# Optimization experiments

Measured on AMD Instinct MI355X. Metric: run time of the kernel, lower is better.

## Reference

```python
import jax, jax.numpy as jnp
import numpy as np

EMBED_DIM = 64
B, H, S, D = 2, 16, 2048, EMBED_DIM


def setup_inputs() -> dict:
    key = jax.random.key(0)
    ks = jax.random.split(key, 5)
    shp = (B, H, S, D)
    return {
        "Q": jax.random.normal(ks[0], shp, dtype=jnp.float32),
        "K": jax.random.normal(ks[1], shp, dtype=jnp.float32),
        "V": jax.random.normal(ks[2], shp, dtype=jnp.float32),
        "Q_position": jax.random.normal(ks[3], shp, dtype=jnp.float32),
        "K_position": jax.random.normal(ks[4], shp, dtype=jnp.float32),
    }


def reference(Q, K, V, Q_position, K_position):
    scale = 1.0 / np.sqrt(EMBED_DIM).astype(np.float32)
    # content scores + positional similarity, both scaled by 1/sqrt(d)
    scores = jnp.einsum("bhqd,bhkd->bhqk", Q, K) * scale
    scores = scores + jnp.einsum("bhqd,bhkd->bhqk", Q_position, K_position) * scale
    attn = jax.nn.softmax(scores, axis=-1)
    context = jnp.einsum("bhqk,bhkd->bhqd", attn, V)
    return context
```

## Files before the change

kernel.cpp:

```cpp
#include <hip/hip_runtime.h>

#define BH_ 32
#define S_ 2048
#define D_ 64
#define DQK 128
#define BQ 256

typedef unsigned short u16;
typedef unsigned int u32;
typedef u16 u16x8 __attribute__((ext_vector_type(8)));
typedef u32 u32x4 __attribute__((ext_vector_type(4)));
typedef __bf16 bf16x8 __attribute__((ext_vector_type(8)));
typedef float f32x16 __attribute__((ext_vector_type(16)));

__device__ __forceinline__ u16 f2bf_rne(float f) {
  unsigned u = __builtin_bit_cast(unsigned, f);
  u += 0x7fffu + ((u >> 16) & 1u);
  return (u16)(u >> 16);
}
__device__ __forceinline__ bf16x8 ld8(const u16* p) {
  return __builtin_bit_cast(bf16x8, *(const u16x8*)p);
}
__device__ __forceinline__ void g2l16(const u16* g, u16* l) {
  __builtin_amdgcn_global_load_lds(
      (const __attribute__((address_space(1))) unsigned int*)g,
      (__attribute__((address_space(3))) unsigned int*)l, 16, 0, 0);
}
__device__ __forceinline__ u32 cvtpk(float lo, float hi) {
  u32 r;
  asm("v_cvt_pk_bf16_f32 %0, %1, %2" : "=v"(r) : "v"(lo), "v"(hi));
  return r;
}
__device__ __forceinline__ void swap32(u32& a, u32& b) {
  asm("v_permlane32_swap_b32 %0, %1" : "+v"(a), "+v"(b));
}
__device__ __forceinline__ f32x16 zero16() {
  f32x16 z;
  #pragma unroll
  for (int i = 0; i < 16; ++i) z[i] = 0.f;
  return z;
}

#define COEF 0.1803368801111204f

__global__ __launch_bounds__(256)
void prep_kernel(const float* __restrict__ K, const float* __restrict__ V,
                 const float* __restrict__ Kp,
                 u16* __restrict__ Kc, u16* __restrict__ Vt) {
  __shared__ float Ls[64][65];
  int b = blockIdx.x;
  if (b < 4096) {
    int t = b * 256 + threadIdx.x;
    int kv    = t & 63;
    int chunk = (t >> 6) & 15;
    int kt    = (t >> 10) & 31;
    int bh    = t >> 15;
    int s     = kt * 64 + kv;
    int col8  = chunk * 8;
    const float* src = (col8 < 64) ? (K  + ((size_t)bh * S_ + s) * D_ + col8)
                                   : (Kp + ((size_t)bh * S_ + s) * D_ + (col8 - 64));
    float4 v0 = *(const float4*)src;
    float4 v1 = *(const float4*)(src + 4);
    u16x8 w;
    w[0] = f2bf_rne(v0.x); w[1] = f2bf_rne(v0.y); w[2] = f2bf_rne(v0.z); w[3] = f2bf_rne(v0.w);
    w[4] = f2bf_rne(v1.x); w[5] = f2bf_rne(v1.y); w[6] = f2bf_rne(v1.z); w[7] = f2bf_rne(v1.w);
    *(u16x8*)(Kc + ((((size_t)bh * 32 + kt) * 16 + chunk) * 64 + kv) * 8) = w;
  } else {
    int id = b - 4096;
    int bh = id >> 5, kt = id & 31;
    int tid = threadIdx.x;
    #pragma unroll
    for (int it = 0; it < 4; ++it) {
      int i = it * 256 + tid;
      int kv = i >> 4, dg = (i & 15) * 4;
      float4 v = *(const float4*)(V + ((size_t)bh * S_ + kt * 64 + kv) * D_ + dg);
      Ls[kv][dg + 0] = v.x; Ls[kv][dg + 1] = v.y;
      Ls[kv][dg + 2] = v.z; Ls[kv][dg + 3] = v.w;
    }
    __syncthreads();
    int d = tid >> 2, kvg = (tid & 3) * 16;
    u16x8 w0, w1;
    #pragma unroll
    for (int j = 0; j < 8; ++j) w0[j] = f2bf_rne(Ls[kvg + j][d]);
    #pragma unroll
    for (int j = 0; j < 8; ++j) w1[j] = f2bf_rne(Ls[kvg + 8 + j][d]);
    u16* base = Vt + ((size_t)bh * 32 + kt) * 4096;
    int c = (tid & 3) * 2;
    *(u16x8*)(base + ((size_t)(c * 64 + d)) * 8)       = w0;
    *(u16x8*)(base + ((size_t)((c + 1) * 64 + d)) * 8) = w1;
  }
}

template <int SPLIT>
__global__ __launch_bounds__(256, 2)
void fa3_kernel(const float* __restrict__ Q, const float* __restrict__ Qp,
                const u16* __restrict__ Kc, const u16* __restrict__ Vtg,
                float* __restrict__ out, float* __restrict__ Opart,
                float* __restrict__ lpart) {
  __shared__ alignas(16) u16 Ks[3][8192];
  __shared__ alignas(16) u16 Vs[3][4096];

  const int tid  = threadIdx.x;
  const int wave = tid >> 6;
  const int lane = tid & 63;
  const int l32  = lane & 31;
  const int hi   = lane >> 5;

  const int id   = blockIdx.x;
  const int p    = SPLIT ? (id & 63) : (id & 31);
  const int qblk = SPLIT ? (id >> 6) : (id >> 5);
  const int bh   = p & 31;
  const int kz   = SPLIT ? (p >> 5) : 0;

  const int qw = qblk * BQ + wave * 64;
  const int kt0 = kz * 16;
  const int NKT = SPLIT ? 16 : 32;

  bf16x8 bq[2][8];
  #pragma unroll
  for (int g = 0; g < 2; ++g)
    #pragma unroll
    for (int kstep = 0; kstep < 8; ++kstep) {
      int k0 = kstep * 16 + hi * 8;
      const float* src = (k0 < 64)
          ? (Q  + ((size_t)bh * S_ + qw + g * 32 + l32) * D_ + k0)
          : (Qp + ((size_t)bh * S_ + qw + g * 32 + l32) * D_ + (k0 - 64));
      float4 v0 = *(const float4*)src;
      float4 v1 = *(const float4*)(src + 4);
      u16x8 w;
      w[0] = f2bf_rne(v0.x * COEF); w[1] = f2bf_rne(v0.y * COEF);
      w[2] = f2bf_rne(v0.z * COEF); w[3] = f2bf_rne(v0.w * COEF);
      w[4] = f2bf_rne(v1.x * COEF); w[5] = f2bf_rne(v1.y * COEF);
      w[6] = f2bf_rne(v1.z * COEF); w[7] = f2bf_rne(v1.w * COEF);
      bq[g][kstep] = __builtin_bit_cast(bf16x8, w);
    }

  const u16* kcp = Kc  + ((size_t)bh * 32 + kt0) * 8192 + tid * 8;
  const u16* vtp = Vtg + ((size_t)bh * 32 + kt0) * 4096 + tid * 8;

  #pragma unroll
  for (int j = 0; j < 4; ++j) g2l16(kcp + j * 2048, &Ks[0][0] + tid * 8 + j * 2048);
  #pragma unroll
  for (int j = 0; j < 2; ++j) g2l16(vtp + j * 2048, &Vs[0][0] + tid * 8 + j * 2048);
  #pragma unroll
  for (int j = 0; j < 4; ++j) g2l16(kcp + 8192 + j * 2048, &Ks[1][0] + tid * 8 + j * 2048);
  #pragma unroll
  for (int j = 0; j < 2; ++j) g2l16(vtp + 4096 + j * 2048, &Vs[1][0] + tid * 8 + j * 2048);

  f32x16 accd[2][2];
  #pragma unroll
  for (int g = 0; g < 2; ++g) { accd[g][0] = zero16(); accd[g][1] = zero16(); }
  float l_part[2] = {0.f, 0.f};

  int cur = 0;
  for (int kt = 0; kt < NKT; ++kt) {
    if (kt == NKT - 1) asm volatile("s_waitcnt vmcnt(0)" ::: "memory");
    else               asm volatile("s_waitcnt vmcnt(6)" ::: "memory");
    __builtin_amdgcn_s_barrier();
    if (kt + 2 < NKT) {
      int nx = cur + 2; if (nx >= 3) nx -= 3;
      const u16* kg = kcp + (size_t)(kt + 2) * 8192;
      u16* kl = &Ks[nx][0] + tid * 8;
      #pragma unroll
      for (int j = 0; j < 4; ++j) g2l16(kg + j * 2048, kl + j * 2048);
      const u16* vg = vtp + (size_t)(kt + 2) * 4096;
      u16* vl = &Vs[nx][0] + tid * 8;
      #pragma unroll
      for (int j = 0; j < 2; ++j) g2l16(vg + j * 2048, vl + j * 2048);
    }
    __builtin_amdgcn_sched_barrier(0);

    const u16* ksb = &Ks[cur][0];
    const u16* vsb = &Vs[cur][0];

    f32x16 s[2][2];
    #pragma unroll
    for (int g = 0; g < 2; ++g) { s[g][0] = zero16(); s[g][1] = zero16(); }
    #pragma unroll
    for (int kstep = 0; kstep < 8; ++kstep) {
      bf16x8 akA = ld8(ksb + (((kstep * 2 + hi) * 64) + l32) * 8);
      bf16x8 akB = ld8(ksb + (((kstep * 2 + hi) * 64) + 32 + l32) * 8);
      #pragma unroll
      for (int g = 0; g < 2; ++g) {
        s[g][0] = __builtin_amdgcn_mfma_f32_32x32x16_bf16(akA, bq[g][kstep], s[g][0], 0, 0, 0);
        s[g][1] = __builtin_amdgcn_mfma_f32_32x32x16_bf16(akB, bq[g][kstep], s[g][1], 0, 0, 0);
      }
    }

    #pragma unroll
    for (int h = 0; h < 2; ++h) {
      #pragma unroll
      for (int g = 0; g < 2; ++g) {
        float rs0 = 0.f, rs1 = 0.f;
        #pragma unroll
        for (int r = 0; r < 8; ++r) {
          float e0 = __builtin_amdgcn_exp2f(s[g][h][r]);
          float e1 = __builtin_amdgcn_exp2f(s[g][h][8 + r]);
          s[g][h][r] = e0; s[g][h][8 + r] = e1;
          rs0 += e0; rs1 += e1;
        }
        l_part[g] += rs0 + rs1;
      }
      #pragma unroll
      for (int k2 = 0; k2 < 2; ++k2) {
        bf16x8 pa[2];
        #pragma unroll
        for (int g = 0; g < 2; ++g) {
          u32 a0 = cvtpk(s[g][h][8 * k2 + 0], s[g][h][8 * k2 + 1]);
          u32 b0 = cvtpk(s[g][h][8 * k2 + 4], s[g][h][8 * k2 + 5]);
          swap32(a0, b0);
          u32 a1 = cvtpk(s[g][h][8 * k2 + 2], s[g][h][8 * k2 + 3]);
          u32 b1 = cvtpk(s[g][h][8 * k2 + 6], s[g][h][8 * k2 + 7]);
          swap32(a1, b1);
          u32x4 pw; pw[0] = a0; pw[1] = a1; pw[2] = b0; pw[3] = b1;
          pa[g] = __builtin_bit_cast(bf16x8, pw);
        }
        int ksl = 2 * h + k2;
        #pragma unroll
        for (int dt = 0; dt < 2; ++dt) {
          bf16x8 bv = ld8(vsb + (((ksl * 2 + hi) * 64) + dt * 32 + l32) * 8);
          #pragma unroll
          for (int g = 0; g < 2; ++g)
            accd[g][dt] = __builtin_amdgcn_mfma_f32_32x32x16_bf16(pa[g], bv, accd[g][dt], 0, 0, 0);
        }
      }
    }
    cur = (cur == 2) ? 0 : cur + 1;
  }

  #pragma unroll
  for (int g = 0; g < 2; ++g) {
    float lsum = l_part[g] + __shfl_xor(l_part[g], 32);
    if (SPLIT) {
      #pragma unroll
      for (int r = 0; r < 16; ++r) {
        int qrow = (r & 3) + 8 * (r >> 2) + 4 * hi;
        size_t rowb = ((size_t)kz * 65536 + (size_t)bh * S_ + qw + g * 32 + qrow) * D_;
        Opart[rowb + l32]      = accd[g][0][r];
        Opart[rowb + 32 + l32] = accd[g][1][r];
      }
      if (hi == 0)
        lpart[(size_t)kz * 65536 + (size_t)bh * S_ + qw + g * 32 + l32] = lsum;
    } else {
      #pragma unroll
      for (int r = 0; r < 16; ++r) {
        int qrow = (r & 3) + 8 * (r >> 2) + 4 * hi;
        float inv = 1.0f / __shfl(lsum, qrow);
        size_t rowb = ((size_t)bh * S_ + qw + g * 32 + qrow) * D_;
        out[rowb + l32]      = accd[g][0][r] * inv;
        out[rowb + 32 + l32] = accd[g][1][r] * inv;
      }
    }
  }
}

__global__ __launch_bounds__(256)
void combine_kernel(const float* __restrict__ Opart, const float* __restrict__ lpart,
                    float* __restrict__ out) {
  int t = blockIdx.x * 256 + threadIdx.x;
  int row = t >> 4;
  int d4  = (t & 15) * 4;
  float4 o0 = *(const float4*)(Opart + (size_t)row * D_ + d4);
  float4 o1 = *(const float4*)(Opart + (size_t)65536 * D_ + (size_t)row * D_ + d4);
  float inv = 1.0f / (lpart[row] + lpart[65536 + row]);
  float4 o;
  o.x = (o0.x + o1.x) * inv; o.y = (o0.y + o1.y) * inv;
  o.z = (o0.z + o1.z) * inv; o.w = (o0.w + o1.w) * inv;
  *(float4*)(out + (size_t)row * D_ + d4) = o;
}

extern "C" void kernel_launch(void* const* d_in, const int* in_sizes, int n_in,
                              void* d_out, int out_size, void* d_ws, size_t ws_size,
                              hipStream_t stream) {
  const float* Q  = (const float*)d_in[0];
  const float* K  = (const float*)d_in[1];
  const float* V  = (const float*)d_in[2];
  const float* Qp = (const float*)d_in[3];
  const float* Kp = (const float*)d_in[4];
  float* out = (float*)d_out;

  const size_t nKc = (size_t)BH_ * S_ * DQK;
  const size_t nVt = (size_t)BH_ * S_ * D_;
  const size_t nO  = (size_t)2 * 65536 * D_;
  const size_t nL  = (size_t)2 * 65536;
  const size_t needSplit = (nO + nL) * 4 + (nKc + nVt) * 2;

  if (ws_size >= needSplit) {
    float* Opart = (float*)d_ws;
    float* lpart = Opart + nO;
    u16* Kc = (u16*)(lpart + nL);
    u16* Vt = Kc + nKc;
    prep_kernel<<<dim3(4096 + 1024), dim3(256), 0, stream>>>(K, V, Kp, Kc, Vt);
    fa3_kernel<1><<<dim3((S_ / BQ) * BH_ * 2), dim3(256), 0, stream>>>(Q, Qp, Kc, Vt, nullptr, Opart, lpart);
    combine_kernel<<<dim3(4096), dim3(256), 0, stream>>>(Opart, lpart, out);
  } else {
    u16* Kc = (u16*)d_ws;
    u16* Vt = Kc + nKc;
    prep_kernel<<<dim3(4096 + 1024), dim3(256), 0, stream>>>(K, V, Kp, Kc, Vt);
    fa3_kernel<0><<<dim3((S_ / BQ) * BH_), dim3(256), 0, stream>>>(Q, Qp, Kc, Vt, out, nullptr, nullptr);
  }
}
```

Before: 176.6 us.

## Interleave exp2 softmax work with MFMA chains and add setprio around matrix phases

Restructures the per-tile inner loop so that the QK^T MFMAs for the second key half run while the exp2 work for the first half executes. The exp2 work for the second half is likewise interleaved with the PV MFMAs of the first half. s_setprio raises wave priority around the pure MFMA phases. The aim is to hide transcendental VALU latency behind matrix-core work instead of running the two phases back to back. This relies on the compiler preserving the interleaving, and the row-sum accumulation order changes slightly.

```diff
diff --git a/kernel.cpp b/kernel.cpp
--- a/kernel.cpp
+++ b/kernel.cpp
@@ -39,6 +39,17 @@
   #pragma unroll
   for (int i = 0; i < 16; ++i) z[i] = 0.f;
   return z;
+}
+__device__ __forceinline__ bf16x8 mkfrag(float s0, float s1, float s2, float s3,
+                                         float s4, float s5, float s6, float s7) {
+  u32 a0 = cvtpk(s0, s1);
+  u32 b0 = cvtpk(s4, s5);
+  swap32(a0, b0);
+  u32 a1 = cvtpk(s2, s3);
+  u32 b1 = cvtpk(s6, s7);
+  swap32(a1, b1);
+  u32x4 pw; pw[0] = a0; pw[1] = a1; pw[2] = b0; pw[3] = b1;
+  return __builtin_bit_cast(bf16x8, pw);
 }
 
 #define COEF 0.1803368801111204f
@@ -173,58 +184,84 @@
     const u16* ksb = &Ks[cur][0];
     const u16* vsb = &Vs[cur][0];
 
-    f32x16 s[2][2];
-    #pragma unroll
-    for (int g = 0; g < 2; ++g) { s[g][0] = zero16(); s[g][1] = zero16(); }
+    f32x16 s0g0 = zero16(), s0g1 = zero16();
+    f32x16 s1g0 = zero16(), s1g1 = zero16();
+    __builtin_amdgcn_s_setprio(1);
     #pragma unroll
     for (int kstep = 0; kstep < 8; ++kstep) {
       bf16x8 akA = ld8(ksb + (((kstep * 2 + hi) * 64) + l32) * 8);
+      s0g0 = __builtin_amdgcn_mfma_f32_32x32x16_bf16(akA, bq[0][kstep], s0g0, 0, 0, 0);
+      s0g1 = __builtin_amdgcn_mfma_f32_32x32x16_bf16(akA, bq[1][kstep], s0g1, 0, 0, 0);
+    }
+    __builtin_amdgcn_s_setprio(0);
+
+    float rs00 = 0.f, rs01 = 0.f, rs10 = 0.f, rs11 = 0.f;
+    #pragma unroll
+    for (int kstep = 0; kstep < 8; ++kstep) {
       bf16x8 akB = ld8(ksb + (((kstep * 2 + hi) * 64) + 32 + l32) * 8);
-      #pragma unroll
-      for (int g = 0; g < 2; ++g) {
-        s[g][0] = __builtin_amdgcn_mfma_f32_32x32x16_bf16(akA, bq[g][kstep], s[g][0], 0, 0, 0);
-        s[g][1] = __builtin_amdgcn_mfma_f32_32x32x16_bf16(akB, bq[g][kstep], s[g][1], 0, 0, 0);
+      s1g0 = __builtin_amdgcn_mfma_f32_32x32x16_bf16(akB, bq[0][kstep], s1g0, 0, 0, 0);
+      s1g1 = __builtin_amdgcn_mfma_f32_32x32x16_bf16(akB, bq[1][kstep], s1g1, 0, 0, 0);
+      const int r0 = kstep * 2, r1 = kstep * 2 + 1;
+      float e;
+      e = __builtin_amdgcn_exp2f(s0g0[r0]); s0g0[r0] = e; rs00 += e;
+      e = __builtin_amdgcn_exp2f(s0g0[r1]); s0g0[r1] = e; rs01 += e;
+      e = __builtin_amdgcn_exp2f(s0g1[r0]); s0g1[r0] = e; rs10 += e;
+      e = __builtin_amdgcn_exp2f(s0g1[r1]); s0g1[r1] = e; rs11 += e;
+    }
+    l_part[0] += rs00 + rs01;
+    l_part[1] += rs10 + rs11;
+
+    bf16x8 paA[2], paB[2];
+    #pragma unroll
+    for (int k2 = 0; k2 < 2; ++k2) {
+      paA[k2] = mkfrag(s0g0[8 * k2 + 0], s0g0[8 * k2 + 1], s0g0[8 * k2 + 2], s0g0[8 * k2 + 3],
+                       s0g0[8 * k2 + 4], s0g0[8 * k2 + 5], s0g0[8 * k2 + 6], s0g0[8 * k2 + 7]);
+      paB[k2] = mkfrag(s0g1[8 * k2 + 0], s0g1[8 * k2 + 1], s0g1[8 * k2 + 2], s0g1[8 * k2 + 3],
+                       s0g1[8 * k2 + 4], s0g1[8 * k2 + 5], s0g1[8 * k2 + 6], s0g1[8 * k2 + 7]);
+    }
+
+    float ts00 = 0.f, ts01 = 0.f, ts10 = 0.f, ts11 = 0.f;
+    #pragma unroll
+    for (int k2 = 0; k2 < 2; ++k2) {
+      #pragma unroll
+      for (int dt = 0; dt < 2; ++dt) {
+        bf16x8 bv = ld8(vsb + (((k2 * 2 + hi) * 64) + dt * 32 + l32) * 8);
+        accd[0][dt] = __builtin_amdgcn_mfma_f32_32x32x16_bf16(paA[k2], bv, accd[0][dt], 0, 0, 0);
+        accd[1][dt] = __builtin_amdgcn_mfma_f32_32x32x16_bf16(paB[k2], bv, accd[1][dt], 0, 0, 0);
+        const int rb = k2 * 8 + dt * 4;
+        float e;
+        e = __builtin_amdgcn_exp2f(s1g0[rb + 0]); s1g0[rb + 0] = e; ts00 += e;
+        e = __builtin_amdgcn_exp2f(s1g0[rb + 1]); s1g0[rb + 1] = e; ts01 += e;
+        e = __builtin_amdgcn_exp2f(s1g0[rb + 2]); s1g0[rb + 2] = e; ts00 += e;
+        e = __builtin_amdgcn_exp2f(s1g0[rb + 3]); s1g0[rb + 3] = e; ts01 += e;
+        e = __builtin_amdgcn_exp2f(s1g1[rb + 0]); s1g1[rb + 0] = e; ts10 += e;
+        e = __builtin_amdgcn_exp2f(s1g1[rb + 1]); s1g1[rb + 1] = e; ts11 += e;
+        e = __builtin_amdgcn_exp2f(s1g1[rb + 2]); s1g1[rb + 2] = e; ts10 += e;
+        e = __builtin_amdgcn_exp2f(s1g1[rb + 3]); s1g1[rb + 3] = e; ts11 += e;
       }
     }
-
-    #pragma unroll
-    for (int h = 0; h < 2; ++h) {
-      #pragma unroll
-      for (int g = 0; g < 2; ++g) {
-        float rs0 = 0.f, rs1 = 0.f;
-        #pragma unroll
-        for (int r = 0; r < 8; ++r) {
-          float e0 = __builtin_amdgcn_exp2f(s[g][h][r]);
-          float e1 = __builtin_amdgcn_exp2f(s[g][h][8 + r]);
-          s[g][h][r] = e0; s[g][h][8 + r] = e1;
-          rs0 += e0; rs1 += e1;
-        }
-        l_part[g] += rs0 + rs1;
+    l_part[0] += ts00 + ts01;
+    l_part[1] += ts10 + ts11;
+
+    #pragma unroll
+    for (int k2 = 0; k2 < 2; ++k2) {
+      paA[k2] = mkfrag(s1g0[8 * k2 + 0], s1g0[8 * k2 + 1], s1g0[8 * k2 + 2], s1g0[8 * k2 + 3],
+                       s1g0[8 * k2 + 4], s1g0[8 * k2 + 5], s1g0[8 * k2 + 6], s1g0[8 * k2 + 7]);
+      paB[k2] = mkfrag(s1g1[8 * k2 + 0], s1g1[8 * k2 + 1], s1g1[8 * k2 + 2], s1g1[8 * k2 + 3],
+                       s1g1[8 * k2 + 4], s1g1[8 * k2 + 5], s1g1[8 * k2 + 6], s1g1[8 * k2 + 7]);
+    }
+    __builtin_amdgcn_s_setprio(1);
+    #pragma unroll
+    for (int k2 = 0; k2 < 2; ++k2) {
+      #pragma unroll
+      for (int dt = 0; dt < 2; ++dt) {
+        bf16x8 bv = ld8(vsb + ((((2 + k2) * 2 + hi) * 64) + dt * 32 + l32) * 8);
+        accd[0][dt] = __builtin_amdgcn_mfma_f32_32x32x16_bf16(paA[k2], bv, accd[0][dt], 0, 0, 0);
+        accd[1][dt] = __builtin_amdgcn_mfma_f32_32x32x16_bf16(paB[k2], bv, accd[1][dt], 0, 0, 0);
       }
-      #pragma unroll
-      for (int k2 = 0; k2 < 2; ++k2) {
-        bf16x8 pa[2];
-        #pragma unroll
-        for (int g = 0; g < 2; ++g) {
-          u32 a0 = cvtpk(s[g][h][8 * k2 + 0], s[g][h][8 * k2 + 1]);
-          u32 b0 = cvtpk(s[g][h][8 * k2 + 4], s[g][h][8 * k2 + 5]);
-          swap32(a0, b0);
-          u32 a1 = cvtpk(s[g][h][8 * k2 + 2], s[g][h][8 * k2 + 3]);
-          u32 b1 = cvtpk(s[g][h][8 * k2 + 6], s[g][h][8 * k2 + 7]);
-          swap32(a1, b1);
-          u32x4 pw; pw[0] = a0; pw[1] = a1; pw[2] = b0; pw[3] = b1;
-          pa[g] = __builtin_bit_cast(bf16x8, pw);
-        }
-        int ksl = 2 * h + k2;
-        #pragma unroll
-        for (int dt = 0; dt < 2; ++dt) {
-          bf16x8 bv = ld8(vsb + (((ksl * 2 + hi) * 64) + dt * 32 + l32) * 8);
-          #pragma unroll
-          for (int g = 0; g < 2; ++g)
-            accd[g][dt] = __builtin_amdgcn_mfma_f32_32x32x16_bf16(pa[g], bv, accd[g][dt], 0, 0, 0);
-        }
-      }
-    }
+    }
+    __builtin_amdgcn_s_setprio(0);
+
     cur = (cur == 2) ? 0 : cur + 1;
   }
 
```

Result: no change. 178.2 us (+0.9%).

## Fuse prep, attention and combine into one cooperative kernel with grid syncs

Applied to the files above, without the earlier changes.

Replaces the three-kernel sequence (K/V bf16 conversion, split-K attention, partial combine) with a single cooperative kernel of 512 blocks that runs the three phases separated by grid-wide syncs. This removes two kernel launch boundaries and their drain/ramp gaps. In exchange, the grid is fixed at 512 blocks with 2 blocks per CU, which caps occupancy and parallelism per phase, and the grid barriers add their own cost. If the cooperative launch fails, it falls back to the old three-kernel path.

```diff
diff --git a/kernel.cpp b/kernel.cpp
--- a/kernel.cpp
+++ b/kernel.cpp
@@ -1,4 +1,7 @@
 #include <hip/hip_runtime.h>
+#include <hip/hip_cooperative_groups.h>
+
+namespace cg = cooperative_groups;
 
 #define BH_ 32
 #define S_ 2048
@@ -42,6 +45,229 @@
 }
 
 #define COEF 0.1803368801111204f
+
+__global__ __launch_bounds__(256, 2)
+void mega_kernel(const float* __restrict__ Q, const float* __restrict__ K,
+                 const float* __restrict__ V, const float* __restrict__ Qp,
+                 const float* __restrict__ Kp,
+                 u16* __restrict__ Kc, u16* __restrict__ Vtg,
+                 float* __restrict__ Opart, float* __restrict__ lpart,
+                 float* __restrict__ out) {
+  __shared__ alignas(16) u16 Ks[3][8192];
+  __shared__ alignas(16) u16 Vs[3][4096];
+
+  const int tid  = threadIdx.x;
+  const int bid  = blockIdx.x;
+  const int gtid = bid * 256 + tid;
+
+  #pragma unroll
+  for (int it = 0; it < 8; ++it) {
+    int t = it * 131072 + gtid;
+    int kv    = t & 63;
+    int chunk = (t >> 6) & 15;
+    int kt    = (t >> 10) & 31;
+    int bh    = t >> 15;
+    int s     = kt * 64 + kv;
+    int col8  = chunk * 8;
+    const float* src = (col8 < 64) ? (K  + ((size_t)bh * S_ + s) * D_ + col8)
+                                   : (Kp + ((size_t)bh * S_ + s) * D_ + (col8 - 64));
+    float4 v0 = *(const float4*)src;
+    float4 v1 = *(const float4*)(src + 4);
+    u16x8 w;
+    w[0] = f2bf_rne(v0.x); w[1] = f2bf_rne(v0.y); w[2] = f2bf_rne(v0.z); w[3] = f2bf_rne(v0.w);
+    w[4] = f2bf_rne(v1.x); w[5] = f2bf_rne(v1.y); w[6] = f2bf_rne(v1.z); w[7] = f2bf_rne(v1.w);
+    *(u16x8*)(Kc + ((((size_t)bh * 32 + kt) * 16 + chunk) * 64 + kv) * 8) = w;
+  }
+
+  {
+    float (*Ls)[65] = reinterpret_cast<float(*)[65]>(&Ks[0][0]);
+    #pragma unroll
+    for (int rep = 0; rep < 2; ++rep) {
+      int idt = bid * 2 + rep;
+      int bh = idt >> 5, kt = idt & 31;
+      __syncthreads();
+      #pragma unroll
+      for (int it = 0; it < 4; ++it) {
+        int i = it * 256 + tid;
+        int kv = i >> 4, dg = (i & 15) * 4;
+        float4 v = *(const float4*)(V + ((size_t)bh * S_ + kt * 64 + kv) * D_ + dg);
+        Ls[kv][dg + 0] = v.x; Ls[kv][dg + 1] = v.y;
+        Ls[kv][dg + 2] = v.z; Ls[kv][dg + 3] = v.w;
+      }
+      __syncthreads();
+      int d = tid >> 2, kvg = (tid & 3) * 16;
+      u16x8 w0, w1;
+      #pragma unroll
+      for (int j = 0; j < 8; ++j) w0[j] = f2bf_rne(Ls[kvg + j][d]);
+      #pragma unroll
+      for (int j = 0; j < 8; ++j) w1[j] = f2bf_rne(Ls[kvg + 8 + j][d]);
+      u16* base = Vtg + ((size_t)bh * 32 + kt) * 4096;
+      int c = (tid & 3) * 2;
+      *(u16x8*)(base + ((size_t)(c * 64 + d)) * 8)       = w0;
+      *(u16x8*)(base + ((size_t)((c + 1) * 64 + d)) * 8) = w1;
+    }
+  }
+
+  cg::this_grid().sync();
+
+  {
+    const int wave = tid >> 6;
+    const int lane = tid & 63;
+    const int l32  = lane & 31;
+    const int hi   = lane >> 5;
+
+    const int p    = bid & 63;
+    const int qblk = bid >> 6;
+    const int bh   = p & 31;
+    const int kz   = p >> 5;
+
+    const int qw = qblk * BQ + wave * 64;
+    const int kt0 = kz * 16;
+    const int NKT = 16;
+
+    bf16x8 bq[2][8];
+    #pragma unroll
+    for (int g = 0; g < 2; ++g)
+      #pragma unroll
+      for (int kstep = 0; kstep < 8; ++kstep) {
+        int k0 = kstep * 16 + hi * 8;
+        const float* src = (k0 < 64)
+            ? (Q  + ((size_t)bh * S_ + qw + g * 32 + l32) * D_ + k0)
+            : (Qp + ((size_t)bh * S_ + qw + g * 32 + l32) * D_ + (k0 - 64));
+        float4 v0 = *(const float4*)src;
+        float4 v1 = *(const float4*)(src + 4);
+        u16x8 w;
+        w[0] = f2bf_rne(v0.x * COEF); w[1] = f2bf_rne(v0.y * COEF);
+        w[2] = f2bf_rne(v0.z * COEF); w[3] = f2bf_rne(v0.w * COEF);
+        w[4] = f2bf_rne(v1.x * COEF); w[5] = f2bf_rne(v1.y * COEF);
+        w[6] = f2bf_rne(v1.z * COEF); w[7] = f2bf_rne(v1.w * COEF);
+        bq[g][kstep] = __builtin_bit_cast(bf16x8, w);
+      }
+
+    const u16* kcp = Kc  + ((size_t)bh * 32 + kt0) * 8192 + tid * 8;
+    const u16* vtp = Vtg + ((size_t)bh * 32 + kt0) * 4096 + tid * 8;
+
+    #pragma unroll
+    for (int j = 0; j < 4; ++j) g2l16(kcp + j * 2048, &Ks[0][0] + tid * 8 + j * 2048);
+    #pragma unroll
+    for (int j = 0; j < 2; ++j) g2l16(vtp + j * 2048, &Vs[0][0] + tid * 8 + j * 2048);
+    #pragma unroll
+    for (int j = 0; j < 4; ++j) g2l16(kcp + 8192 + j * 2048, &Ks[1][0] + tid * 8 + j * 2048);
+    #pragma unroll
+    for (int j = 0; j < 2; ++j) g2l16(vtp + 4096 + j * 2048, &Vs[1][0] + tid * 8 + j * 2048);
+
+    f32x16 accd[2][2];
+    #pragma unroll
+    for (int g = 0; g < 2; ++g) { accd[g][0] = zero16(); accd[g][1] = zero16(); }
+    float l_part[2] = {0.f, 0.f};
+
+    int cur = 0;
+    for (int kt = 0; kt < NKT; ++kt) {
+      if (kt == NKT - 1) asm volatile("s_waitcnt vmcnt(0)" ::: "memory");
+      else               asm volatile("s_waitcnt vmcnt(6)" ::: "memory");
+      __builtin_amdgcn_s_barrier();
+      if (kt + 2 < NKT) {
+        int nx = cur + 2; if (nx >= 3) nx -= 3;
+        const u16* kg = kcp + (size_t)(kt + 2) * 8192;
+        u16* kl = &Ks[nx][0] + tid * 8;
+        #pragma unroll
+        for (int j = 0; j < 4; ++j) g2l16(kg + j * 2048, kl + j * 2048);
+        const u16* vg = vtp + (size_t)(kt + 2) * 4096;
+        u16* vl = &Vs[nx][0] + tid * 8;
+        #pragma unroll
+        for (int j = 0; j < 2; ++j) g2l16(vg + j * 2048, vl + j * 2048);
+      }
+      __builtin_amdgcn_sched_barrier(0);
+
+      const u16* ksb = &Ks[cur][0];
+      const u16* vsb = &Vs[cur][0];
+
+      f32x16 s[2][2];
+      #pragma unroll
+      for (int g = 0; g < 2; ++g) { s[g][0] = zero16(); s[g][1] = zero16(); }
+      #pragma unroll
+      for (int kstep = 0; kstep < 8; ++kstep) {
+        bf16x8 akA = ld8(ksb + (((kstep * 2 + hi) * 64) + l32) * 8);
+        bf16x8 akB = ld8(ksb + (((kstep * 2 + hi) * 64) + 32 + l32) * 8);
+        #pragma unroll
+        for (int g = 0; g < 2; ++g) {
+          s[g][0] = __builtin_amdgcn_mfma_f32_32x32x16_bf16(akA, bq[g][kstep], s[g][0], 0, 0, 0);
+          s[g][1] = __builtin_amdgcn_mfma_f32_32x32x16_bf16(akB, bq[g][kstep], s[g][1], 0, 0, 0);
+        }
+      }
+
+      #pragma unroll
+      for (int h = 0; h < 2; ++h) {
+        #pragma unroll
+        for (int g = 0; g < 2; ++g) {
+          float rs0 = 0.f, rs1 = 0.f;
+          #pragma unroll
+          for (int r = 0; r < 8; ++r) {
+            float e0 = __builtin_amdgcn_exp2f(s[g][h][r]);
+            float e1 = __builtin_amdgcn_exp2f(s[g][h][8 + r]);
+            s[g][h][r] = e0; s[g][h][8 + r] = e1;
+            rs0 += e0; rs1 += e1;
+          }
+          l_part[g] += rs0 + rs1;
+        }
+        #pragma unroll
+        for (int k2 = 0; k2 < 2; ++k2) {
+          bf16x8 pa[2];
+          #pragma unroll
+          for (int g = 0; g < 2; ++g) {
+            u32 a0 = cvtpk(s[g][h][8 * k2 + 0], s[g][h][8 * k2 + 1]);
+            u32 b0 = cvtpk(s[g][h][8 * k2 + 4], s[g][h][8 * k2 + 5]);
+            swap32(a0, b0);
+            u32 a1 = cvtpk(s[g][h][8 * k2 + 2], s[g][h][8 * k2 + 3]);
+            u32 b1 = cvtpk(s[g][h][8 * k2 + 6], s[g][h][8 * k2 + 7]);
+            swap32(a1, b1);
+            u32x4 pw; pw[0] = a0; pw[1] = a1; pw[2] = b0; pw[3] = b1;
+            pa[g] = __builtin_bit_cast(bf16x8, pw);
+          }
+          int ksl = 2 * h + k2;
+          #pragma unroll
+          for (int dt = 0; dt < 2; ++dt) {
+            bf16x8 bv = ld8(vsb + (((ksl * 2 + hi) * 64) + dt * 32 + l32) * 8);
+            #pragma unroll
+            for (int g = 0; g < 2; ++g)
+              accd[g][dt] = __builtin_amdgcn_mfma_f32_32x32x16_bf16(pa[g], bv, accd[g][dt], 0, 0, 0);
+          }
+        }
+      }
+      cur = (cur == 2) ? 0 : cur + 1;
+    }
+
+    #pragma unroll
+    for (int g = 0; g < 2; ++g) {
+      float lsum = l_part[g] + __shfl_xor(l_part[g], 32);
+      #pragma unroll
+      for (int r = 0; r < 16; ++r) {
+        int qrow = (r & 3) + 8 * (r >> 2) + 4 * hi;
+        size_t rowb = ((size_t)kz * 65536 + (size_t)bh * S_ + qw + g * 32 + qrow) * D_;
+        Opart[rowb + l32]      = accd[g][0][r];
+        Opart[rowb + 32 + l32] = accd[g][1][r];
+      }
+      if (hi == 0)
+        lpart[(size_t)kz * 65536 + (size_t)bh * S_ + qw + g * 32 + l32] = lsum;
+    }
+  }
+
+  cg::this_grid().sync();
+
+  #pragma unroll
+  for (int it = 0; it < 8; ++it) {
+    int t = it * 131072 + gtid;
+    int row = t >> 4;
+    int d4  = (t & 15) * 4;
+    float4 o0 = *(const float4*)(Opart + (size_t)row * D_ + d4);
+    float4 o1 = *(const float4*)(Opart + (size_t)65536 * D_ + (size_t)row * D_ + d4);
+    float inv = 1.0f / (lpart[row] + lpart[65536 + row]);
+    float4 o;
+    o.x = (o0.x + o1.x) * inv; o.y = (o0.y + o1.y) * inv;
+    o.z = (o0.z + o1.z) * inv; o.w = (o0.w + o1.w) * inv;
+    *(float4*)(out + (size_t)row * D_ + d4) = o;
+  }
+}
 
 __global__ __launch_bounds__(256)
 void prep_kernel(const float* __restrict__ K, const float* __restrict__ V,
@@ -290,9 +516,18 @@
     float* lpart = Opart + nO;
     u16* Kc = (u16*)(lpart + nL);
     u16* Vt = Kc + nKc;
-    prep_kernel<<<dim3(4096 + 1024), dim3(256), 0, stream>>>(K, V, Kp, Kc, Vt);
-    fa3_kernel<1><<<dim3((S_ / BQ) * BH_ * 2), dim3(256), 0, stream>>>(Q, Qp, Kc, Vt, nullptr, Opart, lpart);
-    combine_kernel<<<dim3(4096), dim3(256), 0, stream>>>(Opart, lpart, out);
+
+    void* args[] = {(void*)&Q, (void*)&K, (void*)&V, (void*)&Qp, (void*)&Kp,
+                    (void*)&Kc, (void*)&Vt, (void*)&Opart, (void*)&lpart,
+                    (void*)&out};
+    hipError_t e = hipLaunchCooperativeKernel((const void*)mega_kernel,
+                                              dim3(512), dim3(256), args, 0, stream);
+    if (e != hipSuccess) {
+      (void)hipGetLastError();
+      prep_kernel<<<dim3(4096 + 1024), dim3(256), 0, stream>>>(K, V, Kp, Kc, Vt);
+      fa3_kernel<1><<<dim3((S_ / BQ) * BH_ * 2), dim3(256), 0, stream>>>(Q, Qp, Kc, Vt, nullptr, Opart, lpart);
+      combine_kernel<<<dim3(4096), dim3(256), 0, stream>>>(Opart, lpart, out);
+    }
   } else {
     u16* Kc = (u16*)d_ws;
     u16* Vt = Kc + nKc;
```

Result: slower. 321.6 us (+82.1%).

## Fuse split-K combine into attention kernel via per-tile atomic counter

Applied to the files above, without the earlier changes.

Removes the separate combine kernel. Each split-K block writes its partial O and row sums, then bumps an atomic counter for its (bh, qblk) pair. The second block to finish reads the other half's partials and writes the normalized output directly. This saves a kernel launch and a full reread and rewrite of the partial buffers, at the cost of a threadfence, extra syncthreads and an atomic per block. The flags are reset inside the prep kernel.

```diff
diff --git a/kernel.cpp b/kernel.cpp
--- a/kernel.cpp
+++ b/kernel.cpp
@@ -46,9 +46,11 @@
 __global__ __launch_bounds__(256)
 void prep_kernel(const float* __restrict__ K, const float* __restrict__ V,
                  const float* __restrict__ Kp,
-                 u16* __restrict__ Kc, u16* __restrict__ Vt) {
+                 u16* __restrict__ Kc, u16* __restrict__ Vt,
+                 int* __restrict__ flags) {
   __shared__ float Ls[64][65];
   int b = blockIdx.x;
+  if (b == 0 && flags != nullptr) flags[threadIdx.x] = 0;
   if (b < 4096) {
     int t = b * 256 + threadIdx.x;
     int kv    = t & 63;
@@ -96,7 +98,7 @@
 void fa3_kernel(const float* __restrict__ Q, const float* __restrict__ Qp,
                 const u16* __restrict__ Kc, const u16* __restrict__ Vtg,
                 float* __restrict__ out, float* __restrict__ Opart,
-                float* __restrict__ lpart) {
+                float* __restrict__ lpart, int* __restrict__ flags) {
   __shared__ alignas(16) u16 Ks[3][8192];
   __shared__ alignas(16) u16 Vs[3][4096];
 
@@ -228,10 +230,13 @@
     cur = (cur == 2) ? 0 : cur + 1;
   }
 
-  #pragma unroll
-  for (int g = 0; g < 2; ++g) {
-    float lsum = l_part[g] + __shfl_xor(l_part[g], 32);
-    if (SPLIT) {
+  float lsum[2];
+  #pragma unroll
+  for (int g = 0; g < 2; ++g) lsum[g] = l_part[g] + __shfl_xor(l_part[g], 32);
+
+  if (SPLIT) {
+    #pragma unroll
+    for (int g = 0; g < 2; ++g) {
       #pragma unroll
       for (int r = 0; r < 16; ++r) {
         int qrow = (r & 3) + 8 * (r >> 2) + 4 * hi;
@@ -240,33 +245,47 @@
         Opart[rowb + 32 + l32] = accd[g][1][r];
       }
       if (hi == 0)
-        lpart[(size_t)kz * 65536 + (size_t)bh * S_ + qw + g * 32 + l32] = lsum;
-    } else {
+        lpart[(size_t)kz * 65536 + (size_t)bh * S_ + qw + g * 32 + l32] = lsum[g];
+    }
+    __threadfence();
+    __syncthreads();
+    if (tid == 0) {
+      int pair = bh * (S_ / BQ) + qblk;
+      ((volatile int*)&Vs[0][0])[0] = atomicAdd(&flags[pair], 1);
+    }
+    __syncthreads();
+    int old = ((volatile int*)&Vs[0][0])[0];
+    if (old == 1) {
+      __threadfence();
+      const float* lp = lpart + (size_t)(kz ^ 1) * 65536 + (size_t)bh * S_;
+      #pragma unroll
+      for (int g = 0; g < 2; ++g) {
+        #pragma unroll
+        for (int r = 0; r < 16; ++r) {
+          int qrow = (r & 3) + 8 * (r >> 2) + 4 * hi;
+          float lo  = __shfl(lsum[g], qrow);
+          float lpv = lp[qw + g * 32 + qrow];
+          float inv = 1.0f / (lo + lpv);
+          size_t prow = ((size_t)(kz ^ 1) * 65536 + (size_t)bh * S_ + qw + g * 32 + qrow) * D_;
+          size_t orow = ((size_t)bh * S_ + qw + g * 32 + qrow) * D_;
+          out[orow + l32]      = (accd[g][0][r] + Opart[prow + l32])      * inv;
+          out[orow + 32 + l32] = (accd[g][1][r] + Opart[prow + 32 + l32]) * inv;
+        }
+      }
+    }
+  } else {
+    #pragma unroll
+    for (int g = 0; g < 2; ++g) {
       #pragma unroll
       for (int r = 0; r < 16; ++r) {
         int qrow = (r & 3) + 8 * (r >> 2) + 4 * hi;
-        float inv = 1.0f / __shfl(lsum, qrow);
+        float inv = 1.0f / __shfl(lsum[g], qrow);
         size_t rowb = ((size_t)bh * S_ + qw + g * 32 + qrow) * D_;
         out[rowb + l32]      = accd[g][0][r] * inv;
         out[rowb + 32 + l32] = accd[g][1][r] * inv;
       }
     }
   }
-}
-
-__global__ __launch_bounds__(256)
-void combine_kernel(const float* __restrict__ Opart, const float* __restrict__ lpart,
-                    float* __restrict__ out) {
-  int t = blockIdx.x * 256 + threadIdx.x;
-  int row = t >> 4;
-  int d4  = (t & 15) * 4;
-  float4 o0 = *(const float4*)(Opart + (size_t)row * D_ + d4);
-  float4 o1 = *(const float4*)(Opart + (size_t)65536 * D_ + (size_t)row * D_ + d4);
-  float inv = 1.0f / (lpart[row] + lpart[65536 + row]);
-  float4 o;
-  o.x = (o0.x + o1.x) * inv; o.y = (o0.y + o1.y) * inv;
-  o.z = (o0.z + o1.z) * inv; o.w = (o0.w + o1.w) * inv;
-  *(float4*)(out + (size_t)row * D_ + d4) = o;
 }
 
 extern "C" void kernel_launch(void* const* d_in, const int* in_sizes, int n_in,
@@ -283,20 +302,20 @@
   const size_t nVt = (size_t)BH_ * S_ * D_;
   const size_t nO  = (size_t)2 * 65536 * D_;
   const size_t nL  = (size_t)2 * 65536;
-  const size_t needSplit = (nO + nL) * 4 + (nKc + nVt) * 2;
+  const size_t needSplit = (nO + nL) * 4 + (nKc + nVt) * 2 + 1024;
 
   if (ws_size >= needSplit) {
     float* Opart = (float*)d_ws;
     float* lpart = Opart + nO;
     u16* Kc = (u16*)(lpart + nL);
     u16* Vt = Kc + nKc;
-    prep_kernel<<<dim3(4096 + 1024), dim3(256), 0, stream>>>(K, V, Kp, Kc, Vt);
-    fa3_kernel<1><<<dim3((S_ / BQ) * BH_ * 2), dim3(256), 0, stream>>>(Q, Qp, Kc, Vt, nullptr, Opart, lpart);
-    combine_kernel<<<dim3(4096), dim3(256), 0, stream>>>(Opart, lpart, out);
+    int* flags = (int*)(Vt + nVt);
+    prep_kernel<<<dim3(4096 + 1024), dim3(256), 0, stream>>>(K, V, Kp, Kc, Vt, flags);
+    fa3_kernel<1><<<dim3((S_ / BQ) * BH_ * 2), dim3(256), 0, stream>>>(Q, Qp, Kc, Vt, out, Opart, lpart, flags);
   } else {
     u16* Kc = (u16*)d_ws;
     u16* Vt = Kc + nKc;
-    prep_kernel<<<dim3(4096 + 1024), dim3(256), 0, stream>>>(K, V, Kp, Kc, Vt);
-    fa3_kernel<0><<<dim3((S_ / BQ) * BH_), dim3(256), 0, stream>>>(Q, Qp, Kc, Vt, out, nullptr, nullptr);
+    prep_kernel<<<dim3(4096 + 1024), dim3(256), 0, stream>>>(K, V, Kp, Kc, Vt, nullptr);
+    fa3_kernel<0><<<dim3((S_ / BQ) * BH_), dim3(256), 0, stream>>>(Q, Qp, Kc, Vt, out, nullptr, nullptr, nullptr);
   }
 }
```

Result: slower. 260.3 us (+47.4%).
